# Performance work log

Measured on AMD Instinct MI355X. Metric: run time of the kernel, lower is better.

## Reference

```python
import jax, jax.numpy as jnp
import numpy as np

B, C_IN, H, W = 4, 16, 64, 64
OUT_C, K, STRIDE = 32, 3, 1
NUM_DEG = 6   # numerator coeffs for x^0..x^5 (order[0]+1)
DEN_DEG = 4


def setup_inputs() -> dict:
    key = jax.random.key(0)
    k1, k2, k3 = jax.random.split(key, 3)
    x = jax.random.normal(k1, (B, C_IN, H, W), dtype=jnp.float32)
    nums = 0.1 * jax.random.normal(k2, (OUT_C * C_IN * K * K, NUM_DEG), dtype=jnp.float32)
    denoms = 0.1 * jax.random.normal(k3, (OUT_C * C_IN * K * K, DEN_DEG), dtype=jnp.float32)
    return {"input": x, "nums": nums, "denoms": denoms}


def _ka_conv(x, nums, denoms):
    pad = (K - 1) // 2
    xp = jnp.pad(x, ((0, 0), (0, 0), (pad, pad), (pad, pad)))
    Ho = (x.shape[2] + 2 * pad - K) // STRIDE + 1
    Wo = (x.shape[3] + 2 * pad - K) // STRIDE + 1
    # patches [B, C, K*K, Ho, Wo] ordered (c, ki, kj) to match nums row layout
    patches = jnp.stack(
        [xp[:, :, i:i + STRIDE * Ho:STRIDE, j:j + STRIDE * Wo:STRIDE]
         for i in range(K) for j in range(K)], axis=2)
    M = C_IN * K * K
    patches = patches.reshape(x.shape[0], M, Ho, Wo)
    # powers x^0..x^5 built by cumulative products (grad-safe at x=0)
    pows = [jnp.ones_like(patches)]
    for _ in range(NUM_DEG - 1):
        pows.append(pows[-1] * patches)
    pw = jnp.stack(pows, axis=-1)  # [B, M, Ho, Wo, NUM_DEG]
    a = nums.reshape(OUT_C, M, NUM_DEG)
    b = denoms.reshape(OUT_C, M, DEN_DEG)
    # per-weight rational: P/Q for every (out_channel, weight, position)
    num = jnp.einsum('bmhwp,omp->bomhw', pw, a)
    den = 1.0 + jnp.abs(jnp.einsum('bmhwq,omq->bomhw', pw[..., 1:1 + DEN_DEG], b))
    return jnp.sum(num / den, axis=2)  # [B, OUT_C, Ho, Wo]


def reference(input, nums, denoms):
    return _ka_conv(input, nums, denoms)
```

## Files before the change

kernel.cpp:

```cpp
#include <hip/hip_runtime.h>


constexpr int Bn = 4, Cin = 16, Hh = 64, Ww = 64, Oc = 32, Mtot = 144;

typedef float v2f __attribute__((ext_vector_type(2)));

__global__ __launch_bounds__(256, 4)
void ka_conv_kernel(const float* __restrict__ x,
                    const float* __restrict__ nums,
                    const float* __restrict__ denoms,
                    float* __restrict__ out) {
  const int tid = threadIdx.x;
  const int n   = blockIdx.x;
  const int ht  = n & 7;
  const int o   = __builtin_amdgcn_readfirstlane((n >> 3) & 31);
  const int b   = n >> 8;

  const int w  = tid & 63;
  const int rg = tid >> 6;
  const int h0 = ht * 8 + rg * 2;

  const int  wm   = max(w - 1, 0), wp = min(w + 1, Ww - 1);
  const bool wl   = w > 0, wr = (w + 1) < Ww;
  const int  h_1  = max(h0 - 1, 0);
  const int  h2c  = min(h0 + 2, Hh - 1);
  const bool htv  = h0 > 0, hbv = (h0 + 2) < Hh;
  const bool tl = htv && wl, tr_ = htv && wr;
  const bool bl = hbv && wl, br = hbv && wr;

  v2f acc = {0.f, 0.f};
  const float* __restrict__ xb   = x + (size_t)b * Cin * Hh * Ww;
  const float* __restrict__ anum = nums   + (size_t)o * Mtot * 6;
  const float* __restrict__ bden = denoms + (size_t)o * Mtot * 4;

#define TAP(t, vt, vb) do {                                                    \
    const float a0 = pa[(t)*6 + 0], a1 = pa[(t)*6 + 1], a2 = pa[(t)*6 + 2];    \
    const float a3 = pa[(t)*6 + 3], a4 = pa[(t)*6 + 4], a5 = pa[(t)*6 + 5];    \
    const float c1 = pb[(t)*4 + 0], c2 = pb[(t)*4 + 1];                        \
    const float c3 = pb[(t)*4 + 2], c4 = pb[(t)*4 + 3];                        \
    const v2f v = {(vt), (vb)};                                                \
    v2f num = __builtin_elementwise_fma((v2f){a5, a5}, v, (v2f){a4, a4});      \
    num = __builtin_elementwise_fma(num, v, (v2f){a3, a3});                    \
    num = __builtin_elementwise_fma(num, v, (v2f){a2, a2});                    \
    num = __builtin_elementwise_fma(num, v, (v2f){a1, a1});                    \
    num = __builtin_elementwise_fma(num, v, (v2f){a0, a0});                    \
    v2f dp = __builtin_elementwise_fma((v2f){c4, c4}, v, (v2f){c3, c3});       \
    dp = __builtin_elementwise_fma(dp, v, (v2f){c2, c2});                      \
    dp = __builtin_elementwise_fma(dp, v, (v2f){c1, c1});                      \
    dp = dp * v;                                                               \
    const v2f den = (v2f){1.f, 1.f} + __builtin_elementwise_abs(dp);           \
    const v2f r = {__builtin_amdgcn_rcpf(den.x), __builtin_amdgcn_rcpf(den.y)};\
    acc = __builtin_elementwise_fma(num, r, acc);                              \
  } while (0)

  #pragma unroll 2
  for (int c = 0; c < Cin; ++c) {
    const float* __restrict__ xc = xb + (size_t)c * (Hh * Ww);
    const float* __restrict__ r0 = xc + h_1 * Ww;
    const float* __restrict__ r1 = xc + h0 * Ww;
    const float* __restrict__ r2 = xc + (h0 + 1) * Ww;
    const float* __restrict__ r3 = xc + h2c * Ww;

    float v00 = r0[wm], v01 = r0[w], v02 = r0[wp];
    float v10 = r1[wm], v11 = r1[w], v12 = r1[wp];
    float v20 = r2[wm], v21 = r2[w], v22 = r2[wp];
    float v30 = r3[wm], v31 = r3[w], v32 = r3[wp];
    v00 = tl  ? v00 : 0.f;  v01 = htv ? v01 : 0.f;  v02 = tr_ ? v02 : 0.f;
    v10 = wl  ? v10 : 0.f;                          v12 = wr  ? v12 : 0.f;
    v20 = wl  ? v20 : 0.f;                          v22 = wr  ? v22 : 0.f;
    v30 = bl  ? v30 : 0.f;  v31 = hbv ? v31 : 0.f;  v32 = br  ? v32 : 0.f;

    const float* __restrict__ pa = anum + c * 54;
    const float* __restrict__ pb = bden + c * 36;
    TAP(0, v00, v10);  TAP(1, v01, v11);  TAP(2, v02, v12);
    TAP(3, v10, v20);  TAP(4, v11, v21);  TAP(5, v12, v22);
    TAP(6, v20, v30);  TAP(7, v21, v31);  TAP(8, v22, v32);
  }
#undef TAP

  float* op = out + ((size_t)(b * Oc + o) * Hh + h0) * Ww + w;
  op[0]  = acc.x;
  op[Ww] = acc.y;
}

extern "C" void kernel_launch(void* const* d_in, const int* in_sizes, int n_in,
                              void* d_out, int out_size, void* d_ws, size_t ws_size,
                              hipStream_t stream) {
  const float* x      = (const float*)d_in[0];
  const float* nums   = (const float*)d_in[1];
  const float* denoms = (const float*)d_in[2];
  float* out          = (float*)d_out;
  dim3 grid(Bn * Oc * 8);
  ka_conv_kernel<<<grid, 256, 0, stream>>>(x, nums, denoms, out);
}
```

Baseline: 32.32 us.

## Pre-pad input and interleave coefficients in a prep kernel before conv

Adds a prep kernel that writes a zero-padded 66x66 copy of the input and packs the numerator and denominator coefficients into 12-float records in workspace. The conv kernel then reads the padded rows directly, with no clamping or select masks, and loads its coefficients from one contiguous, aligned record per tap instead of two separate arrays. The aim is to cut scalar address arithmetic and load count in the main loop. In exchange it adds a second kernel launch and an extra pass over the input, which is significant for a kernel this short.

```diff
diff --git a/kernel.cpp b/kernel.cpp
--- a/kernel.cpp
+++ b/kernel.cpp
@@ -2,14 +2,41 @@
 
 
 constexpr int Bn = 4, Cin = 16, Hh = 64, Ww = 64, Oc = 32, Mtot = 144;
+constexpr int PW = 66;
+constexpr size_t WSX_FLOATS = (size_t)Bn * Cin * PW * PW;
+constexpr int NREC = Oc * Mtot;
 
 typedef float v2f __attribute__((ext_vector_type(2)));
 
-__global__ __launch_bounds__(256, 4)
-void ka_conv_kernel(const float* __restrict__ x,
+__global__ __launch_bounds__(256)
+void ka_prep_kernel(const float* __restrict__ x,
                     const float* __restrict__ nums,
                     const float* __restrict__ denoms,
-                    float* __restrict__ out) {
+                    float* __restrict__ ws) {
+  const int blk = blockIdx.x;
+  if (blk < Bn * Cin) {
+    const float* __restrict__ xp = x + (size_t)blk * Hh * Ww;
+    float* __restrict__ wp_ = ws + (size_t)blk * PW * PW;
+    for (int i = threadIdx.x; i < PW * PW; i += 256) {
+      const int hp = i / PW, wq = i % PW;
+      const bool in = (hp >= 1) & (hp <= Hh) & (wq >= 1) & (wq <= Ww);
+      wp_[i] = in ? xp[(hp - 1) * Ww + (wq - 1)] : 0.f;
+    }
+  } else {
+    const int idx = (blk - Bn * Cin) * 256 + threadIdx.x;
+    if (idx < NREC) {
+      const float* __restrict__ a = nums + (size_t)idx * 6;
+      const float* __restrict__ c = denoms + (size_t)idx * 4;
+      float* __restrict__ r = ws + WSX_FLOATS + (size_t)idx * 12;
+      r[0] = a[0]; r[1] = a[1]; r[2] = a[2]; r[3] = a[3]; r[4] = a[4]; r[5] = a[5];
+      r[6] = c[0]; r[7] = c[1]; r[8] = c[2]; r[9] = c[3];
+      r[10] = 0.f; r[11] = 0.f;
+    }
+  }
+}
+
+__global__ __launch_bounds__(256, 4)
+void ka_conv_kernel(const float* __restrict__ ws, float* __restrict__ out) {
   const int tid = threadIdx.x;
   const int n   = blockIdx.x;
   const int ht  = n & 7;
@@ -20,24 +47,15 @@
   const int rg = tid >> 6;
   const int h0 = ht * 8 + rg * 2;
 
-  const int  wm   = max(w - 1, 0), wp = min(w + 1, Ww - 1);
-  const bool wl   = w > 0, wr = (w + 1) < Ww;
-  const int  h_1  = max(h0 - 1, 0);
-  const int  h2c  = min(h0 + 2, Hh - 1);
-  const bool htv  = h0 > 0, hbv = (h0 + 2) < Hh;
-  const bool tl = htv && wl, tr_ = htv && wr;
-  const bool bl = hbv && wl, br = hbv && wr;
-
   v2f acc = {0.f, 0.f};
-  const float* __restrict__ xb   = x + (size_t)b * Cin * Hh * Ww;
-  const float* __restrict__ anum = nums   + (size_t)o * Mtot * 6;
-  const float* __restrict__ bden = denoms + (size_t)o * Mtot * 4;
+  const float* __restrict__ xb   = ws + (size_t)b * Cin * PW * PW;
+  const float* __restrict__ coef = ws + WSX_FLOATS + (size_t)o * Mtot * 12;
 
 #define TAP(t, vt, vb) do {                                                    \
-    const float a0 = pa[(t)*6 + 0], a1 = pa[(t)*6 + 1], a2 = pa[(t)*6 + 2];    \
-    const float a3 = pa[(t)*6 + 3], a4 = pa[(t)*6 + 4], a5 = pa[(t)*6 + 5];    \
-    const float c1 = pb[(t)*4 + 0], c2 = pb[(t)*4 + 1];                        \
-    const float c3 = pb[(t)*4 + 2], c4 = pb[(t)*4 + 3];                        \
+    const float* __restrict__ rec = pc + (t) * 12;                             \
+    const float a0 = rec[0], a1 = rec[1], a2 = rec[2];                         \
+    const float a3 = rec[3], a4 = rec[4], a5 = rec[5];                         \
+    const float c1 = rec[6], c2 = rec[7], c3 = rec[8], c4 = rec[9];            \
     const v2f v = {(vt), (vb)};                                                \
     v2f num = __builtin_elementwise_fma((v2f){a5, a5}, v, (v2f){a4, a4});      \
     num = __builtin_elementwise_fma(num, v, (v2f){a3, a3});                    \
@@ -55,26 +73,21 @@
 
   #pragma unroll 2
   for (int c = 0; c < Cin; ++c) {
-    const float* __restrict__ xc = xb + (size_t)c * (Hh * Ww);
-    const float* __restrict__ r0 = xc + h_1 * Ww;
-    const float* __restrict__ r1 = xc + h0 * Ww;
-    const float* __restrict__ r2 = xc + (h0 + 1) * Ww;
-    const float* __restrict__ r3 = xc + h2c * Ww;
+    const float* __restrict__ xc = xb + (size_t)c * (PW * PW);
+    const float* __restrict__ p0 = xc + (h0 + 0) * PW + w;
+    const float* __restrict__ p1 = xc + (h0 + 1) * PW + w;
+    const float* __restrict__ p2 = xc + (h0 + 2) * PW + w;
+    const float* __restrict__ p3 = xc + (h0 + 3) * PW + w;
 
-    float v00 = r0[wm], v01 = r0[w], v02 = r0[wp];
-    float v10 = r1[wm], v11 = r1[w], v12 = r1[wp];
-    float v20 = r2[wm], v21 = r2[w], v22 = r2[wp];
-    float v30 = r3[wm], v31 = r3[w], v32 = r3[wp];
-    v00 = tl  ? v00 : 0.f;  v01 = htv ? v01 : 0.f;  v02 = tr_ ? v02 : 0.f;
-    v10 = wl  ? v10 : 0.f;                          v12 = wr  ? v12 : 0.f;
-    v20 = wl  ? v20 : 0.f;                          v22 = wr  ? v22 : 0.f;
-    v30 = bl  ? v30 : 0.f;  v31 = hbv ? v31 : 0.f;  v32 = br  ? v32 : 0.f;
+    const float x00 = p0[0], x01 = p0[1], x02 = p0[2];
+    const float x10 = p1[0], x11 = p1[1], x12 = p1[2];
+    const float x20 = p2[0], x21 = p2[1], x22 = p2[2];
+    const float x30 = p3[0], x31 = p3[1], x32 = p3[2];
 
-    const float* __restrict__ pa = anum + c * 54;
-    const float* __restrict__ pb = bden + c * 36;
-    TAP(0, v00, v10);  TAP(1, v01, v11);  TAP(2, v02, v12);
-    TAP(3, v10, v20);  TAP(4, v11, v21);  TAP(5, v12, v22);
-    TAP(6, v20, v30);  TAP(7, v21, v31);  TAP(8, v22, v32);
+    const float* __restrict__ pc = coef + (size_t)c * 9 * 12;
+    TAP(0, x00, x10);  TAP(1, x01, x11);  TAP(2, x02, x12);
+    TAP(3, x10, x20);  TAP(4, x11, x21);  TAP(5, x12, x22);
+    TAP(6, x20, x30);  TAP(7, x21, x31);  TAP(8, x22, x32);
   }
 #undef TAP
 
@@ -90,6 +103,11 @@
   const float* nums   = (const float*)d_in[1];
   const float* denoms = (const float*)d_in[2];
   float* out          = (float*)d_out;
-  dim3 grid(Bn * Oc * 8);
-  ka_conv_kernel<<<grid, 256, 0, stream>>>(x, nums, denoms, out);
+  float* ws           = (float*)d_ws;
+
+  const int padBlocks = Bn * Cin;
+  const int recBlocks = (NREC + 255) / 256;
+  ka_prep_kernel<<<padBlocks + recBlocks, 256, 0, stream>>>(x, nums, denoms, ws);
+
+  ka_conv_kernel<<<Bn * Oc * 8, 256, 0, stream>>>(ws, out);
 }
```

Result: slower. 34.29 us (+6.1%).
